# Optimization experiments

Measured on AMD Instinct MI355X. Metric: run time of the kernel, lower is better.

Reference implementation:

```python
import math
import jax, jax.numpy as jnp
import numpy as np

TOP_K = 2
N_EXP = 8
TRAIN_CAPACITY = 1.25
MIN_CAPACITY = 4


def _capacity(num_tokens):
    cap = math.floor(TOP_K * TRAIN_CAPACITY * num_tokens / N_EXP)
    cap += cap % 2
    return max(cap, MIN_CAPACITY)


def _router(x, w_g):
    B, T, D = x.shape
    N = B * T
    C = _capacity(N)  # static: depends only on shapes

    logits = jnp.einsum('btd,ed->bte', x, w_g)            # [B,T,E]
    _, top_idx = jax.lax.top_k(logits, TOP_K)             # [B,T,K]
    probs = jax.nn.softmax(logits, axis=-1).reshape(N, N_EXP)  # [N,E]
    idx = top_idx.reshape(N, TOP_K)                       # [N,K]

    # one-hot expert mask, laid out [K, N, E] as in the torch code
    exp_mask = jax.nn.one_hot(idx, N_EXP, dtype=jnp.int32)      # [N,K,E]
    exp_mask = jnp.transpose(exp_mask, (1, 0, 2))               # [K,N,E]

    # position of each routed token within its expert's queue
    rank = jnp.cumsum(exp_mask.reshape(TOP_K * N, N_EXP), axis=0)
    rank = rank.reshape(TOP_K, N, N_EXP) - 1                    # [K,N,E]

    exp_mask = exp_mask * (rank < C).astype(jnp.int32)          # drop over-capacity
    used_capacity = jnp.sum(exp_mask, axis=(0, 1))              # [E]
    rank_sel = jnp.sum(exp_mask * rank, axis=-1)                # [K,N] int

    idx_kn = jnp.transpose(idx)                                 # [K,N]
    keep = jnp.take_along_axis(exp_mask, idx_kn[:, :, None], axis=2)[..., 0]  # [K,N]
    p_sel = jnp.transpose(jnp.take_along_axis(probs, idx, axis=1))            # [K,N]
    w = keep.astype(probs.dtype) * p_sel                        # [K,N]

    # cb_weight[n, e, c] = sum_k exp_weights[k,n,e] * one_hot(rank_sel)[k,n,c]
    # implemented as a direct scatter-add instead of materializing the
    # O(K*N*E*C) outer product (dropped tokens contribute weight 0).
    tok = jnp.arange(N)
    cb_weight = jnp.zeros((N, N_EXP, C), probs.dtype)
    cb_weight = cb_weight.at[tok[None, :], idx_kn, rank_sel].add(w)
    sec_mask = cb_weight != 0
    return used_capacity, cb_weight, sec_mask


def setup_inputs() -> dict:
    key = jax.random.key(0)
    kx, kw = jax.random.split(key)
    x = jax.random.normal(kx, (2, 2048, 1024), dtype=jnp.float32)
    w_g = jax.random.normal(kw, (8, 1024), dtype=jnp.float32) * 0.02
    return {"x": x, "w_g": w_g}


def reference(x, w_g):
    return _router(x, w_g)
```

## Files before the change

### kernel.cpp

```cpp
#include <hip/hip_runtime.h>

#define N_TOK 4096
#define DIM   1024
#define NE    8
#define CAP   1280
#define EC    (NE * CAP)
#define EC4   (EC / 4)
#define NEC   ((size_t)N_TOK * EC)

typedef float nt_float4 __attribute__((ext_vector_type(4)));

__global__ __launch_bounds__(256) void k_logits(const float* __restrict__ x,
                                                const float* __restrict__ wg,
                                                int* __restrict__ top_idx,
                                                float* __restrict__ top_p) {
    __shared__ float swg[NE * DIM];
    const float4* wg4 = (const float4*)wg;
    float4* swg4 = (float4*)swg;
#pragma unroll
    for (int i = 0; i < 8; ++i) {
        int t = i * 256 + threadIdx.x;
        swg4[t] = wg4[t];
    }
    __syncthreads();

    const int wave = threadIdx.x >> 6;
    const int lane = threadIdx.x & 63;
    const int token = blockIdx.x * 4 + wave;

    const float4* x4 = (const float4*)(x + (size_t)token * DIM);
    float acc[NE];
#pragma unroll
    for (int e = 0; e < NE; ++e) acc[e] = 0.f;

#pragma unroll
    for (int c = 0; c < 4; ++c) {
        float4 xv = x4[c * 64 + lane];
#pragma unroll
        for (int e = 0; e < NE; ++e) {
            float4 wv = swg4[e * 256 + c * 64 + lane];
            acc[e] += xv.x * wv.x + xv.y * wv.y + xv.z * wv.z + xv.w * wv.w;
        }
    }
#pragma unroll
    for (int e = 0; e < NE; ++e) {
        float v = acc[e];
#pragma unroll
        for (int off = 32; off > 0; off >>= 1)
            v += __shfl_xor(v, off, 64);
        acc[e] = v;
    }

    if (lane == 0) {
        float m = acc[0];
#pragma unroll
        for (int e = 1; e < NE; ++e) m = fmaxf(m, acc[e]);
        float pe[NE];
        float s = 0.f;
#pragma unroll
        for (int e = 0; e < NE; ++e) { pe[e] = expf(acc[e] - m); s += pe[e]; }
        float inv = 1.f / s;

        int i1 = 0; float v1 = acc[0];
#pragma unroll
        for (int e = 1; e < NE; ++e) if (acc[e] > v1) { v1 = acc[e]; i1 = e; }
        int i2 = (i1 == 0) ? 1 : 0; float v2 = acc[i2];
#pragma unroll
        for (int e = 0; e < NE; ++e)
            if (e != i1 && acc[e] > v2) { v2 = acc[e]; i2 = e; }

        top_idx[token]         = i1;
        top_idx[N_TOK + token] = i2;
        top_p[token]           = pe[i1] * inv;
        top_p[N_TOK + token]   = pe[i2] * inv;
    }
}

__global__ __launch_bounds__(256) void k_rank(const int* __restrict__ top_idx,
                                              int* __restrict__ dest,
                                              float* __restrict__ used) {
    __shared__ int se[2 * N_TOK];
    __shared__ int wsum[4][NE];
    const int t = threadIdx.x;
    const int lane = t & 63;
    const int wave = t >> 6;

    const int4* ti4 = (const int4*)top_idx;
    int4* se4 = (int4*)se;
#pragma unroll
    for (int i = 0; i < 8; ++i)
        se4[i * 256 + t] = ti4[i * 256 + t];
    __syncthreads();

    int cnt[NE];
#pragma unroll
    for (int e = 0; e < NE; ++e) cnt[e] = 0;
    const int base = t * 32;
#pragma unroll
    for (int jj = 0; jj < 32; ++jj) {
        int v = se[base + jj];
#pragma unroll
        for (int e = 0; e < NE; ++e) cnt[e] += (v == e) ? 1 : 0;
    }

    int incl[NE];
#pragma unroll
    for (int e = 0; e < NE; ++e) {
        int s = cnt[e];
#pragma unroll
        for (int off = 1; off < 64; off <<= 1) {
            int u = __shfl_up(s, off, 64);
            if (lane >= off) s += u;
        }
        incl[e] = s;
        if (lane == 63) wsum[wave][e] = s;
    }
    __syncthreads();

    int excl[NE];
#pragma unroll
    for (int e = 0; e < NE; ++e) {
        int off = 0;
#pragma unroll
        for (int w = 0; w < 4; ++w)
            off += (w < wave) ? wsum[w][e] : 0;
        excl[e] = off + incl[e] - cnt[e];
    }
    if (t < NE) {
        int total = wsum[0][t] + wsum[1][t] + wsum[2][t] + wsum[3][t];
        used[t] = (float)min(total, CAP);
    }

    int run[NE];
#pragma unroll
    for (int e = 0; e < NE; ++e) run[e] = excl[e];
#pragma unroll
    for (int jj = 0; jj < 32; ++jj) {
        int j = base + jj;
        int v = se[j];
        int r = run[0];
#pragma unroll
        for (int e = 1; e < NE; ++e) r = (v == e) ? run[e] : r;
#pragma unroll
        for (int e = 0; e < NE; ++e) run[e] += (v == e) ? 1 : 0;
        dest[j] = (r < CAP) ? (v * CAP + r) : -1;
    }
}

__global__ __launch_bounds__(256) void k_out(const int* __restrict__ dest,
                                             const float* __restrict__ top_p,
                                             const float* __restrict__ used,
                                             float* __restrict__ out) {
    const int n = blockIdx.x;
    const int t = threadIdx.x;
    if (n == 0 && t < NE) out[t] = used[t];

    const int   d0 = dest[n];
    const int   d1 = dest[N_TOK + n];
    const float w0 = top_p[n];
    const float w1 = top_p[N_TOK + n];

    nt_float4* cb = (nt_float4*)(out + 8 + (size_t)n * EC);
    nt_float4* mk = (nt_float4*)(out + 8 + NEC + (size_t)n * EC);

#pragma unroll
    for (int i = 0; i < EC4 / 256; ++i) {
        int v = t + 256 * i;
        int b = 4 * v;
        nt_float4 c, m;
        c.x = (d0 == b)     ? w0 : ((d1 == b)     ? w1 : 0.f);
        c.y = (d0 == b + 1) ? w0 : ((d1 == b + 1) ? w1 : 0.f);
        c.z = (d0 == b + 2) ? w0 : ((d1 == b + 2) ? w1 : 0.f);
        c.w = (d0 == b + 3) ? w0 : ((d1 == b + 3) ? w1 : 0.f);
        m.x = (d0 == b     || d1 == b)     ? 1.f : 0.f;
        m.y = (d0 == b + 1 || d1 == b + 1) ? 1.f : 0.f;
        m.z = (d0 == b + 2 || d1 == b + 2) ? 1.f : 0.f;
        m.w = (d0 == b + 3 || d1 == b + 3) ? 1.f : 0.f;
        __builtin_nontemporal_store(c, &cb[v]);
        __builtin_nontemporal_store(m, &mk[v]);
    }
}

extern "C" void kernel_launch(void* const* d_in, const int* in_sizes, int n_in,
                              void* d_out, int out_size, void* d_ws, size_t ws_size,
                              hipStream_t stream) {
    const float* x  = (const float*)d_in[0];
    const float* wg = (const float*)d_in[1];
    float* out = (float*)d_out;
    char* ws = (char*)d_ws;

    int*   top_idx = (int*)(ws);
    float* top_p   = (float*)(ws + 32768);
    int*   dest    = (int*)(ws + 65536);
    float* used    = (float*)(ws + 98304);

    k_logits<<<N_TOK / 4, 256, 0, stream>>>(x, wg, top_idx, top_p);
    k_rank<<<1, 256, 0, stream>>>(top_idx, dest, used);
    k_out<<<N_TOK, 256, 0, stream>>>(dest, top_p, used, out);
}
```

Before: 381.9 us.

## Replace dense output writer with memset plus sparse scatter of routed weights

Zero-fills the combine-weight and mask outputs with an async memset, then launches a small scatter kernel that writes only the routed token slots. This replaces a per-token kernel that computed and stored every output element with nontemporal vector stores. The goal is to let the runtime fill handle the bulk zero traffic more efficiently and to remove the per-element compare work. It adds an extra memset operation on the stream, and the mask is now derived from a nonzero weight.

```diff
diff --git a/kernel.cpp b/kernel.cpp
--- a/kernel.cpp
+++ b/kernel.cpp
@@ -5,10 +5,7 @@
 #define NE    8
 #define CAP   1280
 #define EC    (NE * CAP)
-#define EC4   (EC / 4)
 #define NEC   ((size_t)N_TOK * EC)
-
-typedef float nt_float4 __attribute__((ext_vector_type(4)));
 
 __global__ __launch_bounds__(256) void k_logits(const float* __restrict__ x,
                                                 const float* __restrict__ wg,
@@ -147,37 +144,19 @@
     }
 }
 
-__global__ __launch_bounds__(256) void k_out(const int* __restrict__ dest,
-                                             const float* __restrict__ top_p,
-                                             const float* __restrict__ used,
-                                             float* __restrict__ out) {
-    const int n = blockIdx.x;
-    const int t = threadIdx.x;
-    if (n == 0 && t < NE) out[t] = used[t];
+__global__ __launch_bounds__(256) void k_scatter(const int* __restrict__ dest,
+                                                 const float* __restrict__ top_p,
+                                                 const float* __restrict__ used,
+                                                 float* __restrict__ out) {
+    const int j = blockIdx.x * 256 + threadIdx.x;
+    if (blockIdx.x == 0 && threadIdx.x < NE) out[threadIdx.x] = used[threadIdx.x];
 
-    const int   d0 = dest[n];
-    const int   d1 = dest[N_TOK + n];
-    const float w0 = top_p[n];
-    const float w1 = top_p[N_TOK + n];
-
-    nt_float4* cb = (nt_float4*)(out + 8 + (size_t)n * EC);
-    nt_float4* mk = (nt_float4*)(out + 8 + NEC + (size_t)n * EC);
-
-#pragma unroll
-    for (int i = 0; i < EC4 / 256; ++i) {
-        int v = t + 256 * i;
-        int b = 4 * v;
-        nt_float4 c, m;
-        c.x = (d0 == b)     ? w0 : ((d1 == b)     ? w1 : 0.f);
-        c.y = (d0 == b + 1) ? w0 : ((d1 == b + 1) ? w1 : 0.f);
-        c.z = (d0 == b + 2) ? w0 : ((d1 == b + 2) ? w1 : 0.f);
-        c.w = (d0 == b + 3) ? w0 : ((d1 == b + 3) ? w1 : 0.f);
-        m.x = (d0 == b     || d1 == b)     ? 1.f : 0.f;
-        m.y = (d0 == b + 1 || d1 == b + 1) ? 1.f : 0.f;
-        m.z = (d0 == b + 2 || d1 == b + 2) ? 1.f : 0.f;
-        m.w = (d0 == b + 3 || d1 == b + 3) ? 1.f : 0.f;
-        __builtin_nontemporal_store(c, &cb[v]);
-        __builtin_nontemporal_store(m, &mk[v]);
+    const int d = dest[j];
+    if (d >= 0) {
+        const int n = j & (N_TOK - 1);
+        const float w = top_p[j];
+        out[8 + (size_t)n * EC + d]       = w;
+        out[8 + NEC + (size_t)n * EC + d] = (w != 0.f) ? 1.f : 0.f;
     }
 }
 
@@ -194,7 +173,9 @@
     int*   dest    = (int*)(ws + 65536);
     float* used    = (float*)(ws + 98304);
 
+    hipMemsetAsync(out, 0, (size_t)(8 + 2 * NEC) * sizeof(float), stream);
+
     k_logits<<<N_TOK / 4, 256, 0, stream>>>(x, wg, top_idx, top_p);
     k_rank<<<1, 256, 0, stream>>>(top_idx, dest, used);
-    k_out<<<N_TOK, 256, 0, stream>>>(dest, top_p, used, out);
+    k_scatter<<<2 * N_TOK / 256, 256, 0, stream>>>(dest, top_p, used, out);
 }
```

Result: faster. 356.4 us (-6.7%).
